# Kernel optimization log

Hardware: AMD Instinct MI355X
Metric: run time of the kernel (lower is better)

Reference implementation:

```python
import jax, jax.numpy as jnp
import numpy as np

EMB_D, N_SLOTS, KEY_D, N_ITER = 768, 8, 128, 5
ATTN_EPS = 1e-8
LN_EPS = 1e-5


def layer_norm(x, g, b):
    mu = jnp.mean(x, axis=-1, keepdims=True)
    var = jnp.mean(jnp.square(x - mu), axis=-1, keepdims=True)
    return (x - mu) * jax.lax.rsqrt(var + LN_EPS) * g + b


def xavier(key, shape):
    fan_in, fan_out = shape[-1], shape[-2] if len(shape) > 1 else shape[-1]
    a = float(np.sqrt(6.0 / (fan_in + fan_out)))
    return jax.random.uniform(key, shape, jnp.float32, -a, a)


def setup_inputs() -> dict:
    key = jax.random.key(0)
    ks = jax.random.split(key, 24)
    B, N = 128, 196
    k = KEY_D
    inp = {
        "features": jax.random.normal(ks[0], (B, N, EMB_D), jnp.float32),
        "slot_noise": jax.random.normal(ks[1], (B, N_SLOTS, k), jnp.float32),
        # LayerNorms
        "ln_in_g": jnp.ones((EMB_D,), jnp.float32), "ln_in_b": jnp.zeros((EMB_D,), jnp.float32),
        "ln_slot_g": jnp.ones((k,), jnp.float32), "ln_slot_b": jnp.zeros((k,), jnp.float32),
        "ln_out_g": jnp.ones((k,), jnp.float32), "ln_out_b": jnp.zeros((k,), jnp.float32),
        "ln_dec_g": jnp.ones((k,), jnp.float32), "ln_dec_b": jnp.zeros((k,), jnp.float32),
        # slot prior
        "mu": xavier(ks[2], (1, 1, k)),
        "log_sigma": xavier(ks[3], (1, 1, k)),
        # projections (torch Linear weight layout: [out, in])
        "Wk": xavier(ks[4], (k, EMB_D)),
        "Wq": xavier(ks[5], (k, k)),
        "Wv": xavier(ks[6], (k, EMB_D)),
        # GRUCell
        "W_ih": jax.random.uniform(ks[7], (3 * k, k), jnp.float32, -1.0/np.sqrt(k), 1.0/np.sqrt(k)),
        "W_hh": jax.random.uniform(ks[8], (3 * k, k), jnp.float32, -1.0/np.sqrt(k), 1.0/np.sqrt(k)),
        "b_ih": jnp.zeros((3 * k,), jnp.float32),
        "b_hh": jnp.zeros((3 * k,), jnp.float32),
        # slot MLP
        "mlp_W1": xavier(ks[9], (k, k)), "mlp_b1": jnp.zeros((k,), jnp.float32),
        "mlp_W2": xavier(ks[10], (k, k)), "mlp_b2": jnp.zeros((k,), jnp.float32),
        # decoder
        "dec_W1": xavier(ks[11], (2 * k, k)), "dec_b1": jnp.zeros((2 * k,), jnp.float32),
        "dec_W2": xavier(ks[12], (EMB_D, 2 * k)), "dec_b2": jnp.zeros((EMB_D,), jnp.float32),
        "dec_W3": xavier(ks[13], (EMB_D, EMB_D)), "dec_b3": jnp.zeros((EMB_D,), jnp.float32),
    }
    return inp


def gru_cell(x, h, W_ih, W_hh, b_ih, b_hh):
    gi = x @ W_ih.T + b_ih  # [*, 3k]
    gh = h @ W_hh.T + b_hh
    ir, iz, inn = jnp.split(gi, 3, axis=-1)
    hr, hz, hn = jnp.split(gh, 3, axis=-1)
    r = jax.nn.sigmoid(ir + hr)
    z = jax.nn.sigmoid(iz + hz)
    n = jnp.tanh(inn + r * hn)
    return (1.0 - z) * n + z * h


def reference(features, slot_noise, ln_in_g, ln_in_b, ln_slot_g, ln_slot_b,
              ln_out_g, ln_out_b, ln_dec_g, ln_dec_b, mu, log_sigma,
              Wk, Wq, Wv, W_ih, W_hh, b_ih, b_hh,
              mlp_W1, mlp_b1, mlp_W2, mlp_b2,
              dec_W1, dec_b1, dec_W2, dec_b2, dec_W3, dec_b3):
    feats_ln = layer_norm(features, ln_in_g, ln_in_b)  # [B,N,E]
    slots = slot_noise * jnp.exp(log_sigma) + mu       # [B,K,D]
    k_proj = (feats_ln @ Wk.T) * (KEY_D ** -0.5)       # [B,N,D]
    v_proj = feats_ln @ Wv.T                           # [B,N,D]

    attn_vis = None
    for _ in range(N_ITER):
        slots_prev = slots
        s_ln = layer_norm(slots, ln_slot_g, ln_slot_b)
        q = s_ln @ Wq.T                                # [B,K,D]
        logits = jnp.einsum('bnd,bkd->bnk', k_proj, q)
        attn_vis = jax.nn.softmax(logits, axis=-1)     # softmax over slots
        attn = attn_vis + ATTN_EPS
        attn = attn / jnp.sum(attn, axis=-2, keepdims=True)  # normalize over tokens
        updates = jnp.einsum('bnk,bnd->bkd', attn, v_proj)
        slots = gru_cell(updates, slots_prev, W_ih, W_hh, b_ih, b_hh)
        h = jax.nn.relu(layer_norm(slots, ln_out_g, ln_out_b) @ mlp_W1.T + mlp_b1)
        slots = slots + (h @ mlp_W2.T + mlp_b2)

    sf = layer_norm(slots, ln_dec_g, ln_dec_b)
    sf = jax.nn.relu(sf @ dec_W1.T + dec_b1)
    sf = jax.nn.relu(sf @ dec_W2.T + dec_b2)
    sf = sf @ dec_W3.T + dec_b3                        # [B,K,E]
    recon = jnp.einsum('bkd,bnk->bnd', sf, attn_vis)   # [B,N,E]
    recon_loss = jnp.mean(jnp.square(recon - features))
    return slots, attn_vis, recon_loss
```

## Files before the change

kernel.cpp:

```cpp
#include <hip/hip_runtime.h>
#include <hip/hip_bf16.h>
#include <math.h>

#define B_    128
#define N_    196
#define E_    768
#define K_    8
#define D_    128
#define BNR   (B_*N_)
#define ITERS 5

#define OFF_PART   0
#define OFF_SDEC   512
#define OFF_WBF    66048
#define OFF_KPBF   639488
#define OFF_VPTBF  2343424
#define OFF_ABF    4178432

typedef __attribute__((ext_vector_type(8))) short bf16x8;
typedef __attribute__((ext_vector_type(4))) float f32x4;

#define MFMA16(a, b, c) __builtin_amdgcn_mfma_f32_16x16x32_bf16(a, b, c, 0, 0, 0)

__device__ __forceinline__ float wave_red_sum64(float v) {
    #pragma unroll
    for (int o = 32; o > 0; o >>= 1) v += __shfl_xor(v, o);
    return v;
}

__device__ __forceinline__ unsigned short f2bf(float v) {
    union { float f; unsigned int u; } c; c.f = v;
    unsigned int u = c.u + 0x7fffu + ((c.u >> 16) & 1u);
    return (unsigned short)(u >> 16);
}

__device__ __forceinline__ void gl_lds16(const void* g, void* l) {
    __builtin_amdgcn_global_load_lds(
        (const __attribute__((address_space(1))) unsigned int*)g,
        (__attribute__((address_space(3))) unsigned int*)l, 16, 0, 0);
}

__device__ __forceinline__ int swz128(int row, int j) {
    return row * 128 + ((((j >> 3) ^ (row & 7))) << 3) + (j & 7);
}
__device__ __forceinline__ int swz256(int row, int j) {
    return row * 256 + ((((j >> 3) ^ (row & 7))) << 3) + (j & 7);
}
__device__ __forceinline__ bf16x8 ldA128(const unsigned short* base, int row, int kq, int ks) {
    int ch = (ks * 4 + kq) ^ (row & 7);
    return *(const bf16x8*)(base + row * 128 + ch * 8);
}
__device__ __forceinline__ bf16x8 ldA256(const unsigned short* base, int row, int kq, int ks) {
    int ch = (ks * 4 + kq) ^ (row & 7);
    return *(const bf16x8*)(base + row * 256 + ch * 8);
}
__device__ __forceinline__ bf16x8 ldW128(const unsigned short* W, int row, int ks, int kq) {
    return *(const bf16x8*)(W + (size_t)row * 128 + ks * 32 + kq * 8);
}

struct WCEnt { const float* s; unsigned short* d; int t0; };
struct WCArgs { WCEnt m[8]; };

__global__ __launch_bounds__(256) void prep_all_k(const float* __restrict__ Wq,
                                                  const float* __restrict__ Wk,
                                                  unsigned short* __restrict__ WMt,
                                                  WCArgs a,
                                                  unsigned short* __restrict__ kpb,
                                                  unsigned short* __restrict__ vpt) {
    __shared__ __align__(16) unsigned short Aq[128 * 128];
    __shared__ __align__(16) unsigned short Bk[128 * 128];
    int bid = blockIdx.x;
    int t = threadIdx.x;
    if (bid < 6) {
        const float s = 0.08838834764831845f;
        int e0 = bid * 128;
        for (int idx = t; idx < 16384; idx += 256) {
            int o = idx >> 7, c = idx & 127;
            Aq[swz128(c, o)] = f2bf(Wq[(size_t)o * 128 + c]);
            Bk[swz128(c, o)] = f2bf(Wk[(size_t)o * 768 + e0 + c] * s);
        }
        __syncthreads();
        int w = t >> 6, l = t & 63;
        int wr = w >> 1, wc = w & 1, fr = l & 15, kq = l >> 4;
        f32x4 acc[4][4];
        #pragma unroll
        for (int mi = 0; mi < 4; ++mi)
            #pragma unroll
            for (int nj = 0; nj < 4; ++nj) acc[mi][nj] = (f32x4){0.f, 0.f, 0.f, 0.f};
        #pragma unroll
        for (int ks = 0; ks < 4; ++ks) {
            bf16x8 af[4], bfr[4];
            #pragma unroll
            for (int mi = 0; mi < 4; ++mi) af[mi] = ldA128(Aq, wr * 64 + mi * 16 + fr, kq, ks);
            #pragma unroll
            for (int nj = 0; nj < 4; ++nj) bfr[nj] = ldA128(Bk, wc * 64 + nj * 16 + fr, kq, ks);
            #pragma unroll
            for (int mi = 0; mi < 4; ++mi)
                #pragma unroll
                for (int nj = 0; nj < 4; ++nj)
                    acc[mi][nj] = MFMA16(af[mi], bfr[nj], acc[mi][nj]);
        }
        #pragma unroll
        for (int mi = 0; mi < 4; ++mi) {
            int rowbase = wr * 64 + mi * 16 + kq * 4;
            #pragma unroll
            for (int nj = 0; nj < 4; ++nj) {
                int col = e0 + wc * 64 + nj * 16 + fr;
                #pragma unroll
                for (int r = 0; r < 4; ++r)
                    WMt[(size_t)(rowbase + r) * 768 + col] = f2bf(acc[mi][nj][r]);
            }
        }
    } else if (bid < 518) {
        int cbid = bid - 6, i = 0;
        #pragma unroll
        for (int j = 1; j < 8; ++j) if (cbid >= a.m[j].t0) i = j;
        int off = (cbid - a.m[i].t0) * 2048 + t * 8;
        const float* s = a.m[i].s + off;
        unsigned short* d = a.m[i].d + off;
        float4 v0 = *(const float4*)s, v1 = *(const float4*)(s + 4);
        ushort4 o0, o1;
        o0.x = f2bf(v0.x); o0.y = f2bf(v0.y); o0.z = f2bf(v0.z); o0.w = f2bf(v0.w);
        o1.x = f2bf(v1.x); o1.y = f2bf(v1.y); o1.z = f2bf(v1.z); o1.w = f2bf(v1.w);
        *(ushort4*)d = o0; *(ushort4*)(d + 4) = o1;
    } else {
        int i = (bid - 518) * 256 + t;
        ushort4 z = {0, 0, 0, 0};
        if (i < 49152) {
            int q = i * 4;
            int b = q / 1536, off = q - b * 1536;
            *(ushort4*)(kpb + ((size_t)b * 208 + 196) * 128 + off) = z;
        } else {
            int c = i - 49152;
            int bd = c / 7, cc = c - bd * 7;
            *(ushort4*)(vpt + (size_t)bd * 224 + 196 + cc * 4) = z;
        }
    }
}

__global__ __launch_bounds__(256) void ln_bf16_k(const float* __restrict__ f,
                                                 const float* __restrict__ g,
                                                 const float* __restrict__ bv,
                                                 unsigned short* __restrict__ out) {
    int wid = blockIdx.x * 4 + (threadIdx.x >> 6);
    int lane = threadIdx.x & 63;
    const float* row = f + (size_t)wid * E_;
    float4 x[3];
    float s = 0.f, s2 = 0.f;
    #pragma unroll
    for (int c = 0; c < 3; ++c) {
        x[c] = *(const float4*)(row + c * 256 + lane * 4);
        s  += x[c].x + x[c].y + x[c].z + x[c].w;
        s2 += x[c].x * x[c].x + x[c].y * x[c].y + x[c].z * x[c].z + x[c].w * x[c].w;
    }
    s  = wave_red_sum64(s);
    s2 = wave_red_sum64(s2);
    float m = s * (1.f / E_);
    float rs = rsqrtf(s2 * (1.f / E_) - m * m + 1e-5f);
    #pragma unroll
    for (int c = 0; c < 3; ++c) {
        float4 g4 = *(const float4*)(g + c * 256 + lane * 4);
        float4 b4 = *(const float4*)(bv + c * 256 + lane * 4);
        ushort4 o;
        o.x = f2bf((x[c].x - m) * rs * g4.x + b4.x);
        o.y = f2bf((x[c].y - m) * rs * g4.y + b4.y);
        o.z = f2bf((x[c].z - m) * rs * g4.z + b4.z);
        o.w = f2bf((x[c].w - m) * rs * g4.w + b4.w);
        *(ushort4*)(out + (size_t)wid * E_ + c * 256 + lane * 4) = o;
    }
}

__global__ __launch_bounds__(512) void mfma_proj_k(const unsigned short* __restrict__ Abf,
                                                   const unsigned short* __restrict__ WMt,
                                                   const unsigned short* __restrict__ Wv_bf,
                                                   unsigned short* __restrict__ kpq_bf,
                                                   unsigned short* __restrict__ vpT_bf) {
    __shared__ __align__(16) unsigned short As[128 * 64];
    __shared__ __align__(16) unsigned short Bs[256 * 64];
    const int t = threadIdx.x, w = t >> 6, l = t & 63;
    const int m0 = blockIdx.x * 128;
    const int wr = w >> 2, wc = w & 3;
    const int fr = l & 15, kq = l >> 4;
    f32x4 acc[4][4];
    #pragma unroll
    for (int mi = 0; mi < 4; ++mi)
        #pragma unroll
        for (int nj = 0; nj < 4; ++nj) acc[mi][nj] = (f32x4){0.f, 0.f, 0.f, 0.f};

    for (int ks = 0; ks < E_; ks += 64) {
        __syncthreads();
        #pragma unroll
        for (int j = 0; j < 2; ++j) {
            int ci = j * 512 + (w << 6) + l;
            int r = ci >> 3, c = ci & 7, cg = c ^ (r & 7);
            gl_lds16(Abf + (size_t)(m0 + r) * E_ + ks + cg * 8,
                     As + (size_t)(j * 512 + (w << 6)) * 8);
        }
        #pragma unroll
        for (int j = 0; j < 4; ++j) {
            int ci = j * 512 + (w << 6) + l;
            int r = ci >> 3, c = ci & 7, cg = c ^ (r & 7);
            const unsigned short* src = (r < 128)
                ? WMt   + (size_t)r * E_ + ks + cg * 8
                : Wv_bf + (size_t)(r - 128) * E_ + ks + cg * 8;
            gl_lds16(src, Bs + (size_t)(j * 512 + (w << 6)) * 8);
        }
        __syncthreads();
        #pragma unroll
        for (int kk = 0; kk < 2; ++kk) {
            bf16x8 af[4], bfr[4];
            #pragma unroll
            for (int mi = 0; mi < 4; ++mi) {
                int rr = wr * 64 + mi * 16 + fr;
                af[mi] = *(const bf16x8*)(As + rr * 64 + (((kk * 4 + kq) ^ (rr & 7))) * 8);
            }
            #pragma unroll
            for (int nj = 0; nj < 4; ++nj) {
                int rr = wc * 64 + nj * 16 + fr;
                bfr[nj] = *(const bf16x8*)(Bs + rr * 64 + (((kk * 4 + kq) ^ (rr & 7))) * 8);
            }
            #pragma unroll
            for (int mi = 0; mi < 4; ++mi)
                #pragma unroll
                for (int nj = 0; nj < 4; ++nj)
                    acc[mi][nj] = MFMA16(af[mi], bfr[nj], acc[mi][nj]);
        }
    }
    __syncthreads();
    if (wc < 2) {
        #pragma unroll
        for (int mi = 0; mi < 4; ++mi) {
            int rowbase = m0 + wr * 64 + mi * 16 + kq * 4;
            #pragma unroll
            for (int r = 0; r < 4; ++r) {
                int m = rowbase + r;
                int b = m / 196, rr = m - b * 196;
                size_t o = ((size_t)b * 208 + rr) * 128;
                #pragma unroll
                for (int nj = 0; nj < 4; ++nj)
                    kpq_bf[o + wc * 64 + nj * 16 + fr] = f2bf(acc[mi][nj][r]);
            }
        }
    } else {
        int dbase = (wc - 2) * 64;
        #pragma unroll
        for (int mi = 0; mi < 4; ++mi) {
            int tok = wr * 64 + mi * 16 + kq * 4;
            #pragma unroll
            for (int nj = 0; nj < 4; ++nj) {
                int d = dbase + nj * 16 + fr;
                ushort4 pk;
                pk.x = f2bf(acc[mi][nj][0]); pk.y = f2bf(acc[mi][nj][1]);
                pk.z = f2bf(acc[mi][nj][2]); pk.w = f2bf(acc[mi][nj][3]);
                *(ushort4*)(Bs + d * 128 + (tok ^ ((d & 7) << 3))) = pk;
            }
        }
    }
    __syncthreads();
    {
        int d = t >> 2, mg = t & 3;
        #pragma unroll
        for (int sc = 0; sc < 4; ++sc) {
            int mstart = mg * 32 + sc * 8;
            int cm = mstart >> 3;
            const unsigned short* src = Bs + d * 128 + ((cm ^ (d & 7)) << 3);
            int g0 = m0 + mstart;
            int b0 = g0 / 196, rr0 = g0 - b0 * 196;
            int b7 = (g0 + 7) / 196;
            if (b0 == b7) {
                unsigned short* dst = vpT_bf + ((size_t)b0 * 128 + d) * 224 + rr0;
                *(ushort4*)(dst)     = *(const ushort4*)(src);
                *(ushort4*)(dst + 4) = *(const ushort4*)(src + 4);
            } else {
                #pragma unroll
                for (int e = 0; e < 8; ++e) {
                    int g = g0 + e;
                    int bb = g / 196, rr = g - bb * 196;
                    vpT_bf[((size_t)bb * 128 + d) * 224 + rr] = src[e];
                }
            }
        }
    }
}

template<int KTOT, int EPI>
__global__ __launch_bounds__(256) void mfma_mlp_k(const unsigned short* __restrict__ A,
                                                  const unsigned short* __restrict__ Bw,
                                                  const float* __restrict__ bias,
                                                  unsigned short* __restrict__ out_bf,
                                                  float* __restrict__ out_f,
                                                  int ldN) {
    __shared__ __align__(16) unsigned short As[128 * 64];
    __shared__ __align__(16) unsigned short Bs[128 * 64];
    const int t = threadIdx.x, w = t >> 6, l = t & 63;
    const int m0 = blockIdx.x * 128;
    const int n0 = blockIdx.y * 128;
    const int wr = w >> 1, wc = w & 1;
    const int fr = l & 15, kq = l >> 4;
    f32x4 acc[4][4];
    #pragma unroll
    for (int mi = 0; mi < 4; ++mi)
        #pragma unroll
        for (int nj = 0; nj < 4; ++nj) acc[mi][nj] = (f32x4){0.f, 0.f, 0.f, 0.f};

    for (int ks = 0; ks < KTOT; ks += 64) {
        __syncthreads();
        #pragma unroll
        for (int j = 0; j < 4; ++j) {
            int ci = (w << 8) + (j << 6) + l;
            int r = ci >> 3, c = ci & 7;
            int cg = c ^ (r & 7);
            gl_lds16(A  + (size_t)(m0 + r) * KTOT + ks + cg * 8,
                     As + (size_t)((w << 8) + (j << 6)) * 8);
            gl_lds16(Bw + (size_t)(n0 + r) * KTOT + ks + cg * 8,
                     Bs + (size_t)((w << 8) + (j << 6)) * 8);
        }
        __syncthreads();
        #pragma unroll
        for (int kk = 0; kk < 2; ++kk) {
            bf16x8 af[4], bfr[4];
            int ch = (kk * 4 + kq) ^ (fr & 7);
            #pragma unroll
            for (int mi = 0; mi < 4; ++mi)
                af[mi] = *(const bf16x8*)(As + (wr * 64 + mi * 16 + fr) * 64 + ch * 8);
            #pragma unroll
            for (int nj = 0; nj < 4; ++nj)
                bfr[nj] = *(const bf16x8*)(Bs + (wc * 64 + nj * 16 + fr) * 64 + ch * 8);
            #pragma unroll
            for (int mi = 0; mi < 4; ++mi)
                #pragma unroll
                for (int nj = 0; nj < 4; ++nj)
                    acc[mi][nj] = MFMA16(af[mi], bfr[nj], acc[mi][nj]);
        }
    }
    #pragma unroll
    for (int mi = 0; mi < 4; ++mi) {
        int rowbase = m0 + wr * 64 + mi * 16 + kq * 4;
        #pragma unroll
        for (int nj = 0; nj < 4; ++nj) {
            int col = n0 + wc * 64 + nj * 16 + fr;
            float bc = bias[col];
            #pragma unroll
            for (int r = 0; r < 4; ++r) {
                float v = acc[mi][nj][r] + bc;
                if (EPI == 0)
                    out_bf[(size_t)(rowbase + r) * ldN + col] = f2bf(fmaxf(v, 0.f));
                else
                    out_f[(size_t)(rowbase + r) * ldN + col] = v;
            }
        }
    }
}

__global__ __launch_bounds__(512, 2) void slot_iter_mfma(
    const float* __restrict__ noise,
    const float* __restrict__ lsg, const float* __restrict__ lsb,
    const float* __restrict__ log_, const float* __restrict__ lob,
    const float* __restrict__ ldg_, const float* __restrict__ ldb_,
    const float* __restrict__ mup, const float* __restrict__ lsig,
    const unsigned short* __restrict__ Wih_bf,
    const unsigned short* __restrict__ Whh_bf,
    const float* __restrict__ bih, const float* __restrict__ bhh,
    const unsigned short* __restrict__ W1_bf, const float* __restrict__ mb1,
    const unsigned short* __restrict__ W2_bf, const float* __restrict__ mb2,
    const unsigned short* __restrict__ kpq_bf,
    const unsigned short* __restrict__ vpT_bf,
    float* __restrict__ out_slots, float* __restrict__ out_attn,
    unsigned short* __restrict__ sdec_bf) {

    __shared__ float slots[8][128];
    __shared__ float colpart[8][8];
    __shared__ __align__(16) unsigned short sln_bf[2048];
    __shared__ __align__(16) unsigned short upd_bf[2048];
    __shared__ __align__(16) unsigned short slots_bf[2048];
    __shared__ __align__(16) unsigned short h_bf[2048];
    __shared__ __align__(16) unsigned short attnT_bf[4096];

    const int b = blockIdx.x, t = threadIdx.x;
    const int lane = t & 63, w = t >> 6;
    const int fr = lane & 15, kq = lane >> 4;

    for (int i = t; i < 2048; i += 512) {
        sln_bf[i] = 0; upd_bf[i] = 0; slots_bf[i] = 0; h_bf[i] = 0;
    }
    for (int i = t; i < 4096; i += 512) attnT_bf[i] = 0;

    for (int idx = t; idx < 1024; idx += 512) {
        int k = idx >> 7, d = idx & 127;
        float v = noise[(size_t)b * 1024 + idx] * expf(lsig[d]) + mup[d];
        slots[k][d] = v;
        slots_bf[swz128(k, d)] = f2bf(v);
    }

    bf16x8 kpq_r[2][4];
    #pragma unroll
    for (int p = 0; p < 2; ++p)
        #pragma unroll
        for (int ks = 0; ks < 4; ++ks) kpq_r[p][ks] = (bf16x8){0,0,0,0,0,0,0,0};
    #pragma unroll
    for (int p = 0; p < 2; ++p) {
        int tt = w + p * 8;
        if (tt <= 12) {
            const unsigned short* kpr = kpq_bf + ((size_t)b * 208 + tt * 16 + fr) * 128;
            #pragma unroll
            for (int ks = 0; ks < 4; ++ks)
                kpq_r[p][ks] = *(const bf16x8*)(kpr + ks * 32 + kq * 8);
        }
    }
    bf16x8 vpt_r[7];
    {
        const unsigned short* vpr = vpT_bf + ((size_t)b * 128 + w * 16 + fr) * 224;
        #pragma unroll
        for (int ks = 0; ks < 7; ++ks)
            vpt_r[ks] = *(const bf16x8*)(vpr + ks * 32 + kq * 8);
    }
    bf16x8 w1_r[4], w2_r[4];
    #pragma unroll
    for (int ks = 0; ks < 4; ++ks) {
        w1_r[ks] = ldW128(W1_bf, w * 16 + fr, ks, kq);
        w2_r[ks] = ldW128(W2_bf, w * 16 + fr, ks, kq);
    }
    __syncthreads();

    for (int it = 0; it < ITERS; ++it) {
        bool last = (it == ITERS - 1);
        {
            float x0 = slots[w][lane], x1 = slots[w][lane + 64];
            float s  = wave_red_sum64(x0 + x1);
            float s2 = wave_red_sum64(x0 * x0 + x1 * x1);
            float m = s * 0.0078125f;
            float rs = rsqrtf(s2 * 0.0078125f - m * m + 1e-5f);
            sln_bf[swz128(w, lane)]      = f2bf((x0 - m) * rs * lsg[lane]      + lsb[lane]);
            sln_bf[swz128(w, lane + 64)] = f2bf((x1 - m) * rs * lsg[lane + 64] + lsb[lane + 64]);
        }
        __syncthreads();
        {
            float cp = 0.f;
            #pragma unroll
            for (int p = 0; p < 2; ++p) {
                int tt = w + p * 8;
                if (tt <= 12) {
                    f32x4 acc = {0.f, 0.f, 0.f, 0.f};
                    #pragma unroll
                    for (int ks = 0; ks < 4; ++ks)
                        acc = MFMA16(kpq_r[p][ks], ldA128(sln_bf, fr, kq, ks), acc);
                    #pragma unroll
                    for (int r = 0; r < 4; ++r) {
                        float v = acc[r];
                        float mx = fmaxf(v, __shfl_xor(v, 1));
                        mx = fmaxf(mx, __shfl_xor(mx, 2));
                        mx = fmaxf(mx, __shfl_xor(mx, 4));
                        float e = expf(v - mx);
                        float sm = e;
                        sm += __shfl_xor(sm, 1); sm += __shfl_xor(sm, 2); sm += __shfl_xor(sm, 4);
                        float a = e / sm;
                        int tok = tt * 16 + kq * 4 + r;
                        bool valid = (tok < 196);
                        if (fr < 8 && valid) {
                            attnT_bf[swz256(fr, tok)] = f2bf(a);
                            if (last) out_attn[((size_t)b * 196 + tok) * 8 + fr] = a;
                        }
                        cp += valid ? a : 0.f;
                    }
                }
            }
            cp += __shfl_xor(cp, 16);
            cp += __shfl_xor(cp, 32);
            if (lane < 8) colpart[w][lane] = cp;
        }
        __syncthreads();
        {
            f32x4 acc = {0.f, 0.f, 0.f, 0.f};
            #pragma unroll
            for (int ks = 0; ks < 7; ++ks)
                acc = MFMA16(ldA256(attnT_bf, fr, kq, ks), vpt_r[ks], acc);
            if (kq < 2) {
                #pragma unroll
                for (int r = 0; r < 4; ++r) {
                    int k = kq * 4 + r;
                    float cs = colpart[0][k] + colpart[1][k] + colpart[2][k] + colpart[3][k]
                             + colpart[4][k] + colpart[5][k] + colpart[6][k] + colpart[7][k]
                             + 196.0f * 1e-8f;
                    upd_bf[swz128(k, w * 16 + fr)] = f2bf(acc[r] / cs);
                }
            }
        }
        __syncthreads();
        {
            f32x4 gi0 = {0,0,0,0}, gi1 = {0,0,0,0}, gi2 = {0,0,0,0};
            f32x4 gh0 = {0,0,0,0}, gh1 = {0,0,0,0}, gh2 = {0,0,0,0};
            #pragma unroll
            for (int ks = 0; ks < 4; ++ks) {
                bf16x8 au = ldA128(upd_bf,   fr, kq, ks);
                bf16x8 as = ldA128(slots_bf, fr, kq, ks);
                gi0 = MFMA16(au, ldW128(Wih_bf,       w * 16 + fr, ks, kq), gi0);
                gi1 = MFMA16(au, ldW128(Wih_bf, 128 + w * 16 + fr, ks, kq), gi1);
                gi2 = MFMA16(au, ldW128(Wih_bf, 256 + w * 16 + fr, ks, kq), gi2);
                gh0 = MFMA16(as, ldW128(Whh_bf,       w * 16 + fr, ks, kq), gh0);
                gh1 = MFMA16(as, ldW128(Whh_bf, 128 + w * 16 + fr, ks, kq), gh1);
                gh2 = MFMA16(as, ldW128(Whh_bf, 256 + w * 16 + fr, ks, kq), gh2);
            }
            if (kq < 2) {
                int d = w * 16 + fr;
                float bi0 = bih[d], bi1 = bih[128 + d], bi2 = bih[256 + d];
                float bh0 = bhh[d], bh1 = bhh[128 + d], bh2 = bhh[256 + d];
                #pragma unroll
                for (int r = 0; r < 4; ++r) {
                    int m = kq * 4 + r;
                    float rr = 1.f / (1.f + expf(-((gi0[r] + bi0) + (gh0[r] + bh0))));
                    float zz = 1.f / (1.f + expf(-((gi1[r] + bi1) + (gh1[r] + bh1))));
                    float nn = tanhf((gi2[r] + bi2) + rr * (gh2[r] + bh2));
                    float h = slots[m][d];
                    slots[m][d] = (1.f - zz) * nn + zz * h;
                }
            }
        }
        __syncthreads();
        {
            float x0 = slots[w][lane], x1 = slots[w][lane + 64];
            float s  = wave_red_sum64(x0 + x1);
            float s2 = wave_red_sum64(x0 * x0 + x1 * x1);
            float m = s * 0.0078125f;
            float rs = rsqrtf(s2 * 0.0078125f - m * m + 1e-5f);
            sln_bf[swz128(w, lane)]      = f2bf((x0 - m) * rs * log_[lane]      + lob[lane]);
            sln_bf[swz128(w, lane + 64)] = f2bf((x1 - m) * rs * log_[lane + 64] + lob[lane + 64]);
        }
        __syncthreads();
        {
            f32x4 acc = {0.f, 0.f, 0.f, 0.f};
            #pragma unroll
            for (int ks = 0; ks < 4; ++ks)
                acc = MFMA16(ldA128(sln_bf, fr, kq, ks), w1_r[ks], acc);
            if (kq < 2) {
                float b1 = mb1[w * 16 + fr];
                #pragma unroll
                for (int r = 0; r < 4; ++r)
                    h_bf[swz128(kq * 4 + r, w * 16 + fr)] = f2bf(fmaxf(acc[r] + b1, 0.f));
            }
        }
        __syncthreads();
        {
            f32x4 acc = {0.f, 0.f, 0.f, 0.f};
            #pragma unroll
            for (int ks = 0; ks < 4; ++ks)
                acc = MFMA16(ldA128(h_bf, fr, kq, ks), w2_r[ks], acc);
            if (kq < 2) {
                float b2 = mb2[w * 16 + fr];
                #pragma unroll
                for (int r = 0; r < 4; ++r) {
                    int m = kq * 4 + r, d = w * 16 + fr;
                    float v = slots[m][d] + acc[r] + b2;
                    slots[m][d] = v;
                    slots_bf[swz128(m, d)] = f2bf(v);
                }
            }
        }
        __syncthreads();
    }
    {
        float x0 = slots[w][lane], x1 = slots[w][lane + 64];
        out_slots[(size_t)b * 1024 + w * 128 + lane]      = x0;
        out_slots[(size_t)b * 1024 + w * 128 + lane + 64] = x1;
        float s  = wave_red_sum64(x0 + x1);
        float s2 = wave_red_sum64(x0 * x0 + x1 * x1);
        float m = s * 0.0078125f;
        float rs = rsqrtf(s2 * 0.0078125f - m * m + 1e-5f);
        sdec_bf[((size_t)b * 8 + w) * 128 + lane]      = f2bf((x0 - m) * rs * ldg_[lane]      + ldb_[lane]);
        sdec_bf[((size_t)b * 8 + w) * 128 + lane + 64] = f2bf((x1 - m) * rs * ldg_[lane + 64] + ldb_[lane + 64]);
    }
}

__global__ __launch_bounds__(256) void recon_loss_k(
    const float* __restrict__ feats, const float* __restrict__ attnv,
    const float* __restrict__ sf, float* __restrict__ partials) {

    __shared__ float sfl[8][768];
    __shared__ float al[49][8];
    __shared__ float wred[4];
    int b = blockIdx.x, qd = blockIdx.y, t = threadIdx.x;
    for (int idx = t; idx < 8 * 768; idx += 256)
        ((float*)sfl)[idx] = sf[(size_t)b * 8 * 768 + idx];
    int n0 = qd * 49;
    for (int idx = t; idx < 49 * 8; idx += 256)
        ((float*)al)[idx] = attnv[((size_t)b * N_ + n0) * 8 + idx];
    __syncthreads();
    float acc = 0.f;
    for (int nl = 0; nl < 49; ++nl) {
        float a0 = al[nl][0], a1 = al[nl][1], a2 = al[nl][2], a3 = al[nl][3];
        float a4 = al[nl][4], a5 = al[nl][5], a6 = al[nl][6], a7 = al[nl][7];
        const float* frow = feats + ((size_t)(b * N_ + n0 + nl)) * E_;
        for (int c = t; c < E_; c += 256) {
            float r = sfl[0][c]*a0 + sfl[1][c]*a1 + sfl[2][c]*a2 + sfl[3][c]*a3
                    + sfl[4][c]*a4 + sfl[5][c]*a5 + sfl[6][c]*a6 + sfl[7][c]*a7;
            float d = r - frow[c];
            acc += d * d;
        }
    }
    acc = wave_red_sum64(acc);
    int lane = t & 63, w = t >> 6;
    if (lane == 0) wred[w] = acc;
    __syncthreads();
    if (t == 0) partials[b * 4 + qd] = wred[0] + wred[1] + wred[2] + wred[3];
}

__global__ __launch_bounds__(512) void loss_final_k(const float* __restrict__ partials,
                                                    float* __restrict__ out) {
    __shared__ float wred[8];
    int t = threadIdx.x;
    float v = partials[t];
    v = wave_red_sum64(v);
    if ((t & 63) == 0) wred[t >> 6] = v;
    __syncthreads();
    if (t == 0) {
        float s = 0.f;
        #pragma unroll
        for (int i = 0; i < 8; ++i) s += wred[i];
        out[0] = s / (float)(B_ * N_ * E_);
    }
}

extern "C" void kernel_launch(void* const* d_in, const int* in_sizes, int n_in,
                              void* d_out, int out_size, void* d_ws, size_t ws_size,
                              hipStream_t stream) {
    (void)in_sizes; (void)n_in; (void)out_size; (void)ws_size;
    const float* feats     = (const float*)d_in[0];
    const float* noise     = (const float*)d_in[1];
    const float* ln_in_g   = (const float*)d_in[2];
    const float* ln_in_b   = (const float*)d_in[3];
    const float* ln_slot_g = (const float*)d_in[4];
    const float* ln_slot_b = (const float*)d_in[5];
    const float* ln_out_g  = (const float*)d_in[6];
    const float* ln_out_b  = (const float*)d_in[7];
    const float* ln_dec_g  = (const float*)d_in[8];
    const float* ln_dec_b  = (const float*)d_in[9];
    const float* mu        = (const float*)d_in[10];
    const float* log_sigma = (const float*)d_in[11];
    const float* Wk        = (const float*)d_in[12];
    const float* Wq        = (const float*)d_in[13];
    const float* Wv        = (const float*)d_in[14];
    const float* W_ih      = (const float*)d_in[15];
    const float* W_hh      = (const float*)d_in[16];
    const float* b_ih      = (const float*)d_in[17];
    const float* b_hh      = (const float*)d_in[18];
    const float* mlp_W1    = (const float*)d_in[19];
    const float* mlp_b1    = (const float*)d_in[20];
    const float* mlp_W2    = (const float*)d_in[21];
    const float* mlp_b2    = (const float*)d_in[22];
    const float* dec_W1    = (const float*)d_in[23];
    const float* dec_b1    = (const float*)d_in[24];
    const float* dec_W2    = (const float*)d_in[25];
    const float* dec_b2    = (const float*)d_in[26];
    const float* dec_W3    = (const float*)d_in[27];
    const float* dec_b3    = (const float*)d_in[28];

    float* ws    = (float*)d_ws;
    float* parts = ws + OFF_PART;
    unsigned short* sdec_bf = (unsigned short*)(ws + OFF_SDEC);
    unsigned short* Wbase   = (unsigned short*)(ws + OFF_WBF);
    unsigned short* Wv_bf   = Wbase;
    unsigned short* Wih_bf  = Wbase + 98304;
    unsigned short* Whh_bf  = Wbase + 147456;
    unsigned short* W1_bf   = Wbase + 196608;
    unsigned short* W2_bf   = Wbase + 212992;
    unsigned short* dW1_bf  = Wbase + 229376;
    unsigned short* dW2_bf  = Wbase + 262144;
    unsigned short* dW3_bf  = Wbase + 458752;
    unsigned short* WMt     = Wbase + 1048576;
    unsigned short* kpq_bf  = (unsigned short*)(ws + OFF_KPBF);
    unsigned short* vpT_bf  = (unsigned short*)(ws + OFF_VPTBF);
    unsigned short* Abf     = (unsigned short*)(ws + OFF_ABF);
    float*          sf      = ws + OFF_ABF;
    unsigned short* h1_bf   = (unsigned short*)(ws + OFF_ABF + 786432);
    unsigned short* h2_bf   = (unsigned short*)(ws + OFF_ABF + 786432 + 131072);

    float* out_slots = (float*)d_out;
    float* out_attn  = out_slots + 131072;
    float* out_loss  = out_slots + 331776;

    WCArgs wa;
    wa.m[0] = {Wv,     Wv_bf,  0};
    wa.m[1] = {W_ih,   Wih_bf, 48};
    wa.m[2] = {W_hh,   Whh_bf, 72};
    wa.m[3] = {mlp_W1, W1_bf,  96};
    wa.m[4] = {mlp_W2, W2_bf,  104};
    wa.m[5] = {dec_W1, dW1_bf, 112};
    wa.m[6] = {dec_W2, dW2_bf, 128};
    wa.m[7] = {dec_W3, dW3_bf, 224};
    prep_all_k<<<1158, 256, 0, stream>>>(Wq, Wk, WMt, wa, kpq_bf, vpT_bf);

    ln_bf16_k<<<BNR / 4, 256, 0, stream>>>(feats, ln_in_g, ln_in_b, Abf);
    mfma_proj_k<<<BNR / 128, 512, 0, stream>>>(Abf, WMt, Wv_bf, kpq_bf, vpT_bf);

    slot_iter_mfma<<<B_, 512, 0, stream>>>(noise, ln_slot_g, ln_slot_b, ln_out_g, ln_out_b,
                                           ln_dec_g, ln_dec_b, mu, log_sigma,
                                           Wih_bf, Whh_bf, b_ih, b_hh,
                                           W1_bf, mlp_b1, W2_bf, mlp_b2, kpq_bf, vpT_bf,
                                           out_slots, out_attn, sdec_bf);

    mfma_mlp_k<128, 0><<<dim3(8, 2), 256, 0, stream>>>(sdec_bf, dW1_bf, dec_b1, h1_bf, nullptr, 256);
    mfma_mlp_k<256, 0><<<dim3(8, 6), 256, 0, stream>>>(h1_bf,  dW2_bf, dec_b2, h2_bf, nullptr, 768);
    mfma_mlp_k<768, 1><<<dim3(8, 6), 256, 0, stream>>>(h2_bf,  dW3_bf, dec_b3, nullptr, sf, 768);

    recon_loss_k<<<dim3(B_, 4), 256, 0, stream>>>(feats, out_attn, sf, parts);
    loss_final_k<<<1, 512, 0, stream>>>(parts, out_loss);
}
```

Baseline: 206.7 us.

## Reload key projections per iteration and normalize attention in shared memory before update GEMM

Stops holding the key-projection fragments in registers across iterations and reloads them from global memory each iteration, cutting register pressure. Occupancy is now requested through amdgpu_waves_per_eu instead of the launch-bounds minimum. Softmax outputs are staged as fp32 in a new shared array, and a separate pass applies the epsilon and column normalization before the bf16 conversion. This adds an extra barrier and pass per iteration and repeated global/L2 loads, in exchange for lower VGPR use and normalization that matches the reference (epsilon added before dividing).

```diff
diff --git a/kernel.cpp b/kernel.cpp
--- a/kernel.cpp
+++ b/kernel.cpp
@@ -352,7 +352,9 @@
     }
 }
 
-__global__ __launch_bounds__(512, 2) void slot_iter_mfma(
+__global__ __launch_bounds__(512)
+__attribute__((amdgpu_waves_per_eu(2, 2)))
+void slot_iter_mfma(
     const float* __restrict__ noise,
     const float* __restrict__ lsg, const float* __restrict__ lsb,
     const float* __restrict__ log_, const float* __restrict__ lob,
@@ -369,6 +371,7 @@
     unsigned short* __restrict__ sdec_bf) {
 
     __shared__ float slots[8][128];
+    __shared__ float attn[208][9];
     __shared__ float colpart[8][8];
     __shared__ __align__(16) unsigned short sln_bf[2048];
     __shared__ __align__(16) unsigned short upd_bf[2048];
@@ -392,21 +395,6 @@
         slots_bf[swz128(k, d)] = f2bf(v);
     }
 
-    bf16x8 kpq_r[2][4];
-    #pragma unroll
-    for (int p = 0; p < 2; ++p)
-        #pragma unroll
-        for (int ks = 0; ks < 4; ++ks) kpq_r[p][ks] = (bf16x8){0,0,0,0,0,0,0,0};
-    #pragma unroll
-    for (int p = 0; p < 2; ++p) {
-        int tt = w + p * 8;
-        if (tt <= 12) {
-            const unsigned short* kpr = kpq_bf + ((size_t)b * 208 + tt * 16 + fr) * 128;
-            #pragma unroll
-            for (int ks = 0; ks < 4; ++ks)
-                kpq_r[p][ks] = *(const bf16x8*)(kpr + ks * 32 + kq * 8);
-        }
-    }
     bf16x8 vpt_r[7];
     {
         const unsigned short* vpr = vpT_bf + ((size_t)b * 128 + w * 16 + fr) * 224;
@@ -441,9 +429,11 @@
                 int tt = w + p * 8;
                 if (tt <= 12) {
                     f32x4 acc = {0.f, 0.f, 0.f, 0.f};
+                    const unsigned short* kpr = kpq_bf + ((size_t)b * 208 + tt * 16 + fr) * 128;
                     #pragma unroll
                     for (int ks = 0; ks < 4; ++ks)
-                        acc = MFMA16(kpq_r[p][ks], ldA128(sln_bf, fr, kq, ks), acc);
+                        acc = MFMA16(*(const bf16x8*)(kpr + ks * 32 + kq * 8),
+                                     ldA128(sln_bf, fr, kq, ks), acc);
                     #pragma unroll
                     for (int r = 0; r < 4; ++r) {
                         float v = acc[r];
@@ -456,10 +446,7 @@
                         float a = e / sm;
                         int tok = tt * 16 + kq * 4 + r;
                         bool valid = (tok < 196);
-                        if (fr < 8 && valid) {
-                            attnT_bf[swz256(fr, tok)] = f2bf(a);
-                            if (last) out_attn[((size_t)b * 196 + tok) * 8 + fr] = a;
-                        }
+                        if (fr < 8 && valid) attn[tok][fr] = a;
                         cp += valid ? a : 0.f;
                     }
                 }
@@ -470,19 +457,28 @@
         }
         __syncthreads();
         {
+            int k = t & 7;
+            float cs = colpart[0][k] + colpart[1][k] + colpart[2][k] + colpart[3][k]
+                     + colpart[4][k] + colpart[5][k] + colpart[6][k] + colpart[7][k]
+                     + 196.0f * 1e-8f;
+            float inv = 1.f / cs;
+            for (int idx = t; idx < 1568; idx += 512) {
+                int n = idx >> 3;
+                float raw = attn[n][k];
+                attnT_bf[swz256(k, n)] = f2bf((raw + 1e-8f) * inv);
+                if (last) out_attn[((size_t)b * 196 + n) * 8 + k] = raw;
+            }
+        }
+        __syncthreads();
+        {
             f32x4 acc = {0.f, 0.f, 0.f, 0.f};
             #pragma unroll
             for (int ks = 0; ks < 7; ++ks)
                 acc = MFMA16(ldA256(attnT_bf, fr, kq, ks), vpt_r[ks], acc);
             if (kq < 2) {
                 #pragma unroll
-                for (int r = 0; r < 4; ++r) {
-                    int k = kq * 4 + r;
-                    float cs = colpart[0][k] + colpart[1][k] + colpart[2][k] + colpart[3][k]
-                             + colpart[4][k] + colpart[5][k] + colpart[6][k] + colpart[7][k]
-                             + 196.0f * 1e-8f;
-                    upd_bf[swz128(k, w * 16 + fr)] = f2bf(acc[r] / cs);
-                }
+                for (int r = 0; r < 4; ++r)
+                    upd_bf[swz128(kq * 4 + r, w * 16 + fr)] = f2bf(acc[r]);
             }
         }
         __syncthreads();
```

Measured after the change: 196.6 us. 4.9% less time.
